# Kernel optimization log

Hardware: AMD Instinct MI355X
Metric: run time of the kernel (lower is better)

The kernel has to match this reference:

```python
import jax, jax.numpy as jnp
import numpy as np

B, D_IN, D_OUT, P = 4096, 1024, 1024, 16


def setup_inputs() -> dict:
    key = jax.random.key(0)
    k_x, k_A, k_b, k_W, k_c = jax.random.split(key, 5)
    return {
        "x": jax.random.normal(k_x, (B, D_IN), dtype=jnp.float32),
        "A": jax.random.normal(k_A, (P, D_IN, D_IN), dtype=jnp.float32),
        "b": jax.random.normal(k_b, (P, D_IN), dtype=jnp.float32),
        "W": jax.random.normal(k_W, (P, D_OUT, D_IN), dtype=jnp.float32),
        "c": jax.random.normal(k_c, (P, D_OUT), dtype=jnp.float32),
    }


def reference(x, A, b, W, c):
    # membership: sigmoid(-sum_k((A[p] x)_k - b[p,k])) == sigmoid(-(x . A[p].sum(rows) - b[p].sum()))
    scores = jnp.einsum("bd,pkd->bp", x, A) - jnp.sum(b, axis=1)  # (B, P)
    m = jax.nn.sigmoid(-scores)
    m = m / (jnp.sum(m, axis=1, keepdims=True) + 1e-6)            # (B, P)
    # combine: sum_p m[b,p] * (x @ W[p].T + c[p])
    out = jnp.einsum("bp,pod,bd->bo", m, W, x) + m @ c            # (B, D_OUT)
    return out
```

## Files before the change

### kernel.cpp

```cpp
#include <hip/hip_runtime.h>
#include <hip/hip_bf16.h>
#include <stdint.h>


typedef __attribute__((ext_vector_type(4))) float f32x4;
typedef __attribute__((ext_vector_type(8))) short bf16x8;

#define WBF_OFF   0u
#define XBF_OFF   33554432u
#define ASUM_OFF  41943040u
#define BSUM_OFF  42008576u
#define M_OFF     42008832u
#define APART_OFF 44040192u
#define PART_OFF  50331648u

__device__ __forceinline__ unsigned short f2bf(float f) {
  unsigned u = __builtin_bit_cast(unsigned, f);
  unsigned r = (u + 0x7fffu + ((u >> 16) & 1u)) >> 16;
  return (unsigned short)r;
}

__device__ __forceinline__ void gload_lds16(const void* g, void* l) {
  __builtin_amdgcn_global_load_lds(
      (const __attribute__((address_space(1))) void*)g,
      (__attribute__((address_space(3))) void*)l, 16, 0, 0);
}

__global__ void asum_part(const float* __restrict__ A, float* __restrict__ apart) {
  const int p = blockIdx.x >> 4, kc = blockIdx.x & 15;
  const int t = threadIdx.x;
  const float4* Ap = (const float4*)(A + (size_t)p * 1048576 + (size_t)kc * 65536);
  float sx = 0.f, sy = 0.f, sz = 0.f, sw = 0.f;
#pragma unroll 8
  for (int k = 0; k < 64; ++k) {
    float4 v = Ap[k * 256 + t];
    sx += v.x; sy += v.y; sz += v.z; sw += v.w;
  }
  ((float4*)apart)[((size_t)kc * 16 + p) * 256 + t] = make_float4(sx, sy, sz, sw);
}

__global__ void asum_final(const float* __restrict__ apart, const float* __restrict__ b,
                           float* __restrict__ Asum, float* __restrict__ bsum) {
  const int p = blockIdx.x;
  const int t = threadIdx.x;
  float4 acc = make_float4(0.f, 0.f, 0.f, 0.f);
#pragma unroll
  for (int kc = 0; kc < 16; ++kc) {
    float4 v = ((const float4*)apart)[((size_t)kc * 16 + p) * 256 + t];
    acc.x += v.x; acc.y += v.y; acc.z += v.z; acc.w += v.w;
  }
  ((float4*)(Asum + p * 1024))[t] = acc;
  float4 bv = ((const float4*)b)[(size_t)p * 256 + t];
  float s = bv.x + bv.y + bv.z + bv.w;
  __shared__ float red[256];
  red[t] = s;
  __syncthreads();
  for (int off = 128; off > 0; off >>= 1) {
    if (t < off) red[t] += red[t + off];
    __syncthreads();
  }
  if (t == 0) bsum[p] = red[0];
}

__global__ void convert_bf16(const float* __restrict__ src,
                             unsigned short* __restrict__ dst, int n4) {
  int i = blockIdx.x * blockDim.x + threadIdx.x;
  const int stride = gridDim.x * blockDim.x;
  for (; i < n4; i += stride) {
    float4 v = ((const float4*)src)[i];
    uint2 o;
    o.x = (unsigned)f2bf(v.x) | ((unsigned)f2bf(v.y) << 16);
    o.y = (unsigned)f2bf(v.z) | ((unsigned)f2bf(v.w) << 16);
    ((uint2*)dst)[i] = o;
  }
}

__global__ void memberships_fused(const float* __restrict__ x, const float* __restrict__ Asum,
                                  const float* __restrict__ bsum, float* __restrict__ m,
                                  unsigned short* __restrict__ xbf) {
  const int wave = threadIdx.x >> 6, lane = threadIdx.x & 63;
  const int b = blockIdx.x * 4 + wave;
  const float4* xrow4 = (const float4*)(x + (size_t)b * 1024);
  float4 xv[4];
#pragma unroll
  for (int i = 0; i < 4; ++i) xv[i] = xrow4[i * 64 + lane];
  ushort4* xbo = (ushort4*)(xbf + (size_t)b * 1024);
#pragma unroll
  for (int i = 0; i < 4; ++i) {
    ushort4 h;
    h.x = f2bf(xv[i].x); h.y = f2bf(xv[i].y);
    h.z = f2bf(xv[i].z); h.w = f2bf(xv[i].w);
    xbo[i * 64 + lane] = h;
  }
  float myE = 0.f, sumE = 0.f;
#pragma unroll
  for (int p = 0; p < 16; ++p) {
    const float4* ap4 = (const float4*)(Asum + p * 1024);
    float s = 0.f;
#pragma unroll
    for (int i = 0; i < 4; ++i) {
      float4 av = ap4[i * 64 + lane];
      s += xv[i].x * av.x + xv[i].y * av.y + xv[i].z * av.z + xv[i].w * av.w;
    }
#pragma unroll
    for (int off = 32; off > 0; off >>= 1) s += __shfl_xor(s, off, 64);
    const float score = s - bsum[p];
    const float e = 1.f / (1.f + __expf(score));
    sumE += e;
    if ((lane & 15) == p) myE = e;
  }
  const float mv = myE / (sumE + 1e-6f);
  if (lane < 16) m[(size_t)b * 16 + lane] = mv;
}

template <int NSLAB>
__global__ __launch_bounds__(256, 2) void moe_gemm(
    const unsigned short* __restrict__ xbf,
    const unsigned short* __restrict__ wbf,
    const float* __restrict__ mptr,
    const float* __restrict__ c,
    float* __restrict__ dst)
{
  __shared__ __align__(16) unsigned char lds[2 * 16384];
  __shared__ __align__(16) float m_lds[128 * 16];

  const int tid = threadIdx.x;
  const int bid = blockIdx.x;
  const int tile = bid & 255;
  const int bt = tile >> 3, ot = tile & 7;
  const int brow = bt << 7, ocol = ot << 7;

  const int sg = (NSLAB == 4) ? ((bid >> 8) & 1) : (NSLAB == 2 ? (bid >> 8) : 0);
  const int kh = (NSLAB == 4) ? (bid >> 9) : 0;
  const int PC = (NSLAB >= 2) ? 8 : 16;
  const int p0 = sg * 8;
  const int KSTEPS = (NSLAB == 4) ? 16 : 32;
  const int kbase = kh * 512;
  const int TOT = PC * KSTEPS;

  const int lane = tid & 63;
  const int wv = tid >> 6;
  const int wr = wv >> 1, wc = wv & 1;

  {
    const float4* msrc = (const float4*)(mptr + (size_t)brow * 16);
    float4* mdst = (float4*)m_lds;
    mdst[tid] = msrc[tid];
    mdst[256 + tid] = msrc[256 + tid];
  }

  auto stage = [&](int buf, int u) {
    const int p = p0 + (u / KSTEPS);
    const int k0 = kbase + (u % KSTEPS) * 32;
    const unsigned short* Ag = xbf + (size_t)brow * 1024 + k0;
    const unsigned short* Bg = wbf + (size_t)p * 1048576 + (size_t)ocol * 1024 + k0;
    unsigned char* base = lds + buf * 16384;
#pragma unroll
    for (int r = 0; r < 4; ++r) {
      const int e = ((r & 1) << 8) + tid;
      const int row = e >> 2, seg = e & 3;
      const unsigned short* g = (r < 2 ? Ag : Bg) + (size_t)row * 1024 + seg * 8;
      unsigned char* l = base + (r >= 2 ? 8192 : 0) +
                         ((((r & 1) << 8) + (tid & ~63)) << 4);
      gload_lds16(g, l);
    }
  };

  auto compute = [&](int buf, f32x4 (&acc)[4][4]) {
    const unsigned char* base = lds + buf * 16384;
    const unsigned char* Ab = base + ((wr * 64 + (lane & 15)) << 6) + ((lane >> 4) << 4);
    const unsigned char* Bb = base + 8192 + ((wc * 64 + (lane & 15)) << 6) + ((lane >> 4) << 4);
    bf16x8 a[4], b[4];
#pragma unroll
    for (int i = 0; i < 4; ++i) {
      a[i] = *(const bf16x8*)(Ab + i * 1024);
      b[i] = *(const bf16x8*)(Bb + i * 1024);
    }
#pragma unroll
    for (int mi = 0; mi < 4; ++mi)
#pragma unroll
      for (int ni = 0; ni < 4; ++ni)
        acc[mi][ni] = __builtin_amdgcn_mfma_f32_16x16x32_bf16(a[mi], b[ni], acc[mi][ni], 0, 0, 0);
  };

  const f32x4 zv = {0.f, 0.f, 0.f, 0.f};
  f32x4 master[4][4];
#pragma unroll
  for (int mi = 0; mi < 4; ++mi)
#pragma unroll
    for (int ni = 0; ni < 4; ++ni) master[mi][ni] = zv;

  int cur = 0;
  stage(0, 0);

  for (int pi = 0; pi < PC; ++pi) {
    const int p = p0 + pi;
    f32x4 acc[4][4];
#pragma unroll
    for (int mi = 0; mi < 4; ++mi)
#pragma unroll
      for (int ni = 0; ni < 4; ++ni) acc[mi][ni] = zv;

#pragma unroll 2
    for (int ks = 0; ks < KSTEPS; ++ks) {
      const int u = pi * KSTEPS + ks;
      __syncthreads();
      if (u + 1 < TOT) stage(cur ^ 1, u + 1);
      compute(cur, acc);
      cur ^= 1;
    }

    float cvn[4] = {0.f, 0.f, 0.f, 0.f};
    if constexpr (NSLAB == 1) {
#pragma unroll
      for (int ni = 0; ni < 4; ++ni)
        cvn[ni] = c[(size_t)p * 1024 + ocol + wc * 64 + ni * 16 + (lane & 15)];
    }
#pragma unroll
    for (int mi = 0; mi < 4; ++mi)
#pragma unroll
      for (int j = 0; j < 4; ++j) {
        const int lrow = wr * 64 + mi * 16 + ((lane >> 4) << 2) + j;
        const float ms = m_lds[lrow * 16 + p];
#pragma unroll
        for (int ni = 0; ni < 4; ++ni) {
          if constexpr (NSLAB == 1) master[mi][ni][j] += ms * (acc[mi][ni][j] + cvn[ni]);
          else                      master[mi][ni][j] += ms * acc[mi][ni][j];
        }
      }
  }

  const int slab = (NSLAB == 4) ? (kh * 2 + sg) : sg;
  float* ob = dst + (size_t)slab * 4194304;
#pragma unroll
  for (int mi = 0; mi < 4; ++mi)
#pragma unroll
    for (int j = 0; j < 4; ++j) {
      const int grow = brow + wr * 64 + mi * 16 + ((lane >> 4) << 2) + j;
#pragma unroll
      for (int ni = 0; ni < 4; ++ni) {
        const int gcol = ocol + wc * 64 + ni * 16 + (lane & 15);
        ob[(size_t)grow * 1024 + gcol] = master[mi][ni][j];
      }
    }
}

template <int NSLAB>
__global__ void reduce_out(const float* __restrict__ part, const float* __restrict__ m,
                           const float* __restrict__ c, float* __restrict__ out) {
  const int b = blockIdx.x;
  const int t = threadIdx.x;
  __shared__ float msh[16];
  if (t < 16) msh[t] = m[(size_t)b * 16 + t];
  __syncthreads();
  const int o = t * 4;
  float rx = 0.f, ry = 0.f, rz = 0.f, rw = 0.f;
#pragma unroll
  for (int s = 0; s < NSLAB; ++s) {
    float4 a = *(const float4*)(part + (size_t)s * 4194304 + (size_t)b * 1024 + o);
    rx += a.x; ry += a.y; rz += a.z; rw += a.w;
  }
#pragma unroll
  for (int p = 0; p < 16; ++p) {
    const float mp = msh[p];
    float4 cv = *(const float4*)(c + (size_t)p * 1024 + o);
    rx += mp * cv.x; ry += mp * cv.y; rz += mp * cv.z; rw += mp * cv.w;
  }
  *(float4*)(out + (size_t)b * 1024 + o) = make_float4(rx, ry, rz, rw);
}

extern "C" void kernel_launch(void* const* d_in, const int* in_sizes, int n_in,
                              void* d_out, int out_size, void* d_ws, size_t ws_size,
                              hipStream_t stream) {
  const float* x = (const float*)d_in[0];
  const float* A = (const float*)d_in[1];
  const float* b = (const float*)d_in[2];
  const float* W = (const float*)d_in[3];
  const float* c = (const float*)d_in[4];
  float* out = (float*)d_out;
  char* ws = (char*)d_ws;

  unsigned short* wbf = (unsigned short*)(ws + WBF_OFF);
  unsigned short* xbf = (unsigned short*)(ws + XBF_OFF);
  float* Asum = (float*)(ws + ASUM_OFF);
  float* bsum = (float*)(ws + BSUM_OFF);
  float* mm = (float*)(ws + M_OFF);
  float* apart = (float*)(ws + APART_OFF);
  float* part = (float*)(ws + PART_OFF);

  asum_part<<<256, 256, 0, stream>>>(A, apart);
  asum_final<<<16, 256, 0, stream>>>(apart, b, Asum, bsum);
  convert_bf16<<<4096, 256, 0, stream>>>(W, wbf, 16777216 / 4);
  memberships_fused<<<1024, 256, 0, stream>>>(x, Asum, bsum, mm, xbf);

  const size_t need4 = (size_t)PART_OFF + 4ull * 16777216ull;
  const size_t need2 = (size_t)PART_OFF + 2ull * 16777216ull;
  if (ws_size >= need4) {
    moe_gemm<4><<<1024, 256, 0, stream>>>(xbf, wbf, mm, c, part);
    reduce_out<4><<<4096, 256, 0, stream>>>(part, mm, c, out);
  } else if (ws_size >= need2) {
    moe_gemm<2><<<512, 256, 0, stream>>>(xbf, wbf, mm, c, part);
    reduce_out<2><<<4096, 256, 0, stream>>>(part, mm, c, out);
  } else {
    moe_gemm<1><<<256, 256, 0, stream>>>(xbf, wbf, mm, c, out);
  }
}
```

Measured before the change: 368.4 us.

## Shrink GEMM output tile to 128x64 and drop K-split slab variant

Changes the moe_gemm block tile from 128x128 to 128x64 output columns, so each wave computes 4x2 MFMA fragments instead of 4x4. The 4-slab K-split path is removed and replaced by a 2-slab expert split with twice as many tiles, keeping the grid at 1024 blocks. The aim is to cut per-block register and LDS use for better occupancy, and to halve partial-sum traffic in reduce_out (2 slabs instead of 4). In exchange, arithmetic intensity per LDS load drops and x tiles are reloaded twice as often across column tiles.

Measured after the change: 526.3 us. +42.8%, slower.

```diff
diff --git a/kernel.cpp b/kernel.cpp
--- a/kernel.cpp
+++ b/kernel.cpp
@@ -121,22 +121,18 @@
     const float* __restrict__ c,
     float* __restrict__ dst)
 {
-  __shared__ __align__(16) unsigned char lds[2 * 16384];
+  __shared__ __align__(16) unsigned char lds[2 * 12288];
   __shared__ __align__(16) float m_lds[128 * 16];
 
   const int tid = threadIdx.x;
   const int bid = blockIdx.x;
-  const int tile = bid & 255;
-  const int bt = tile >> 3, ot = tile & 7;
-  const int brow = bt << 7, ocol = ot << 7;
-
-  const int sg = (NSLAB == 4) ? ((bid >> 8) & 1) : (NSLAB == 2 ? (bid >> 8) : 0);
-  const int kh = (NSLAB == 4) ? (bid >> 9) : 0;
-  const int PC = (NSLAB >= 2) ? 8 : 16;
+  const int sg = (NSLAB == 2) ? (bid >> 9) : 0;
+  const int tile = (NSLAB == 2) ? (bid & 511) : bid;
+  const int bt = tile >> 4, ot = tile & 15;
+  const int brow = bt << 7, ocol = ot << 6;
+  const int PC = (NSLAB == 2) ? 8 : 16;
   const int p0 = sg * 8;
-  const int KSTEPS = (NSLAB == 4) ? 16 : 32;
-  const int kbase = kh * 512;
-  const int TOT = PC * KSTEPS;
+  const int TOT = PC * 32;
 
   const int lane = tid & 63;
   const int wv = tid >> 6;
@@ -150,71 +146,73 @@
   }
 
   auto stage = [&](int buf, int u) {
-    const int p = p0 + (u / KSTEPS);
-    const int k0 = kbase + (u % KSTEPS) * 32;
+    const int p = p0 + (u >> 5);
+    const int k0 = (u & 31) << 5;
     const unsigned short* Ag = xbf + (size_t)brow * 1024 + k0;
     const unsigned short* Bg = wbf + (size_t)p * 1048576 + (size_t)ocol * 1024 + k0;
-    unsigned char* base = lds + buf * 16384;
-#pragma unroll
-    for (int r = 0; r < 4; ++r) {
-      const int e = ((r & 1) << 8) + tid;
-      const int row = e >> 2, seg = e & 3;
-      const unsigned short* g = (r < 2 ? Ag : Bg) + (size_t)row * 1024 + seg * 8;
-      unsigned char* l = base + (r >= 2 ? 8192 : 0) +
-                         ((((r & 1) << 8) + (tid & ~63)) << 4);
+    unsigned char* base = lds + buf * 12288;
+#pragma unroll
+    for (int r = 0; r < 2; ++r) {
+      const int e = (r << 8) + tid;
+      const unsigned short* g = Ag + (size_t)(e >> 2) * 1024 + (e & 3) * 8;
+      unsigned char* l = base + (((r << 8) + (tid & ~63)) << 4);
       gload_lds16(g, l);
     }
+    {
+      const unsigned short* g = Bg + (size_t)(tid >> 2) * 1024 + (tid & 3) * 8;
+      unsigned char* l = base + 8192 + ((tid & ~63) << 4);
+      gload_lds16(g, l);
+    }
   };
 
-  auto compute = [&](int buf, f32x4 (&acc)[4][4]) {
-    const unsigned char* base = lds + buf * 16384;
+  auto compute = [&](int buf, f32x4 (&acc)[4][2]) {
+    const unsigned char* base = lds + buf * 12288;
     const unsigned char* Ab = base + ((wr * 64 + (lane & 15)) << 6) + ((lane >> 4) << 4);
-    const unsigned char* Bb = base + 8192 + ((wc * 64 + (lane & 15)) << 6) + ((lane >> 4) << 4);
-    bf16x8 a[4], b[4];
-#pragma unroll
-    for (int i = 0; i < 4; ++i) {
-      a[i] = *(const bf16x8*)(Ab + i * 1024);
-      b[i] = *(const bf16x8*)(Bb + i * 1024);
-    }
+    const unsigned char* Bb = base + 8192 + ((wc * 32 + (lane & 15)) << 6) + ((lane >> 4) << 4);
+    bf16x8 a[4], b[2];
+#pragma unroll
+    for (int i = 0; i < 4; ++i) a[i] = *(const bf16x8*)(Ab + i * 1024);
+#pragma unroll
+    for (int i = 0; i < 2; ++i) b[i] = *(const bf16x8*)(Bb + i * 1024);
 #pragma unroll
     for (int mi = 0; mi < 4; ++mi)
 #pragma unroll
-      for (int ni = 0; ni < 4; ++ni)
+      for (int ni = 0; ni < 2; ++ni)
         acc[mi][ni] = __builtin_amdgcn_mfma_f32_16x16x32_bf16(a[mi], b[ni], acc[mi][ni], 0, 0, 0);
   };
 
   const f32x4 zv = {0.f, 0.f, 0.f, 0.f};
-  f32x4 master[4][4];
+  f32x4 master[4][2];
 #pragma unroll
   for (int mi = 0; mi < 4; ++mi)
 #pragma unroll
-    for (int ni = 0; ni < 4; ++ni) master[mi][ni] = zv;
+    for (int ni = 0; ni < 2; ++ni) master[mi][ni] = zv;
 
   int cur = 0;
   stage(0, 0);
 
   for (int pi = 0; pi < PC; ++pi) {
     const int p = p0 + pi;
-    f32x4 acc[4][4];
+    f32x4 acc[4][2];
 #pragma unroll
     for (int mi = 0; mi < 4; ++mi)
 #pragma unroll
-      for (int ni = 0; ni < 4; ++ni) acc[mi][ni] = zv;
+      for (int ni = 0; ni < 2; ++ni) acc[mi][ni] = zv;
 
 #pragma unroll 2
-    for (int ks = 0; ks < KSTEPS; ++ks) {
-      const int u = pi * KSTEPS + ks;
+    for (int ks = 0; ks < 32; ++ks) {
+      const int u = pi * 32 + ks;
       __syncthreads();
       if (u + 1 < TOT) stage(cur ^ 1, u + 1);
       compute(cur, acc);
       cur ^= 1;
     }
 
-    float cvn[4] = {0.f, 0.f, 0.f, 0.f};
+    float cvn[2] = {0.f, 0.f};
     if constexpr (NSLAB == 1) {
 #pragma unroll
-      for (int ni = 0; ni < 4; ++ni)
-        cvn[ni] = c[(size_t)p * 1024 + ocol + wc * 64 + ni * 16 + (lane & 15)];
+      for (int ni = 0; ni < 2; ++ni)
+        cvn[ni] = c[(size_t)p * 1024 + ocol + wc * 32 + ni * 16 + (lane & 15)];
     }
 #pragma unroll
     for (int mi = 0; mi < 4; ++mi)
@@ -223,23 +221,22 @@
         const int lrow = wr * 64 + mi * 16 + ((lane >> 4) << 2) + j;
         const float ms = m_lds[lrow * 16 + p];
 #pragma unroll
-        for (int ni = 0; ni < 4; ++ni) {
+        for (int ni = 0; ni < 2; ++ni) {
           if constexpr (NSLAB == 1) master[mi][ni][j] += ms * (acc[mi][ni][j] + cvn[ni]);
           else                      master[mi][ni][j] += ms * acc[mi][ni][j];
         }
       }
   }
 
-  const int slab = (NSLAB == 4) ? (kh * 2 + sg) : sg;
-  float* ob = dst + (size_t)slab * 4194304;
+  float* ob = dst + (size_t)sg * 4194304;
 #pragma unroll
   for (int mi = 0; mi < 4; ++mi)
 #pragma unroll
     for (int j = 0; j < 4; ++j) {
       const int grow = brow + wr * 64 + mi * 16 + ((lane >> 4) << 2) + j;
 #pragma unroll
-      for (int ni = 0; ni < 4; ++ni) {
-        const int gcol = ocol + wc * 64 + ni * 16 + (lane & 15);
+      for (int ni = 0; ni < 2; ++ni) {
+        const int gcol = ocol + wc * 32 + ni * 16 + (lane & 15);
         ob[(size_t)grow * 1024 + gcol] = master[mi][ni][j];
       }
     }
@@ -293,15 +290,11 @@
   convert_bf16<<<4096, 256, 0, stream>>>(W, wbf, 16777216 / 4);
   memberships_fused<<<1024, 256, 0, stream>>>(x, Asum, bsum, mm, xbf);
 
-  const size_t need4 = (size_t)PART_OFF + 4ull * 16777216ull;
   const size_t need2 = (size_t)PART_OFF + 2ull * 16777216ull;
-  if (ws_size >= need4) {
-    moe_gemm<4><<<1024, 256, 0, stream>>>(xbf, wbf, mm, c, part);
-    reduce_out<4><<<4096, 256, 0, stream>>>(part, mm, c, out);
-  } else if (ws_size >= need2) {
-    moe_gemm<2><<<512, 256, 0, stream>>>(xbf, wbf, mm, c, part);
+  if (ws_size >= need2) {
+    moe_gemm<2><<<1024, 256, 0, stream>>>(xbf, wbf, mm, c, part);
     reduce_out<2><<<4096, 256, 0, stream>>>(part, mm, c, out);
   } else {
-    moe_gemm<1><<<256, 256, 0, stream>>>(xbf, wbf, mm, c, out);
-  }
-}
+    moe_gemm<1><<<512, 256, 0, stream>>>(xbf, wbf, mm, c, out);
+  }
+}
```
